# Kernel optimization log

Hardware: AMD Instinct MI355X
Metric: run time of the kernel (lower is better)

The kernel has to match this reference:

```python
import jax, jax.numpy as jnp
import numpy as np
from jax import lax

N, C1, C2, H, W = 4, 256, 256, 80, 80
CH = 128           # c_ = int(c2 * e)
G, KS = 1, 3       # groups, kernel_size
K = KS * KS        # sampling points per group
PAD, DIL = 1, 1
EPS_BN, EPS_LN = 1e-5, 1e-6


def conv_bn_silu(x, w, g, b, m, v, stride=1):
    # ultralytics Conv: conv(bias=False) + BatchNorm2d(eval) + SiLU
    pad = (w.shape[2] - 1) // 2
    y = lax.conv_general_dilated(x, w, (stride, stride), [(pad, pad), (pad, pad)],
                                 dimension_numbers=('NCHW', 'OIHW', 'NCHW'))
    s = g / jnp.sqrt(v + EPS_BN)
    y = y * s[None, :, None, None] + (b - m * s)[None, :, None, None]
    return jax.nn.silu(y)


def dcnv3_core(x, offset, mask):
    # x: (N,H,W,C) NHWC; offset: (N,H,W,G*K*2); mask: (N,H,W,G,K) softmaxed over K
    n, h, w, c = x.shape
    gc = c // G
    xp = jnp.pad(x, ((0, 0), (PAD, PAD), (PAD, PAD), (0, 0)))
    Hp, Wp = h + 2 * PAD, w + 2 * PAD
    base = (DIL * (KS - 1)) // 2
    # reference points (normalized by padded spatial size), stride 1
    ref_x = (jnp.arange(w, dtype=x.dtype) + base + 0.5) / Wp   # (W,)
    ref_y = (jnp.arange(h, dtype=x.dtype) + base + 0.5) / Hp   # (H,)
    gx = (jnp.arange(KS, dtype=x.dtype) * DIL - base) / Wp
    gy = (jnp.arange(KS, dtype=x.dtype) * DIL - base) / Hp
    grid_x = jnp.repeat(gx, KS)   # point p = i*KS + j -> x = gx[i]
    grid_y = jnp.tile(gy, KS)     # y = gy[j]  (torch meshgrid 'ij' ordering)
    off = offset.reshape(n, h, w, G, K, 2)
    loc_x = ref_x[None, None, :, None, None] + grid_x + off[..., 0] / Wp
    loc_y = ref_y[None, :, None, None, None] + grid_y + off[..., 1] / Hp
    # grid_sample align_corners=False: pixel = norm * size - 0.5
    px = loc_x * Wp - 0.5
    py = loc_y * Hp - 0.5
    x0 = jnp.floor(px); y0 = jnp.floor(py)
    lw, lh = px - x0, py - y0
    x0i, y0i = x0.astype(jnp.int32), y0.astype(jnp.int32)
    xv = jnp.transpose(xp.reshape(n, Hp * Wp, G, gc), (0, 2, 1, 3))  # (N,G,S,gc)
    tw = lambda a: jnp.transpose(a, (0, 3, 1, 2, 4))[..., None]      # (N,H,W,G,K)->(N,G,H,W,K,1)

    def gather(yi, xi):
        valid = ((xi >= 0) & (xi < Wp) & (yi >= 0) & (yi < Hp)).astype(x.dtype)
        idx = jnp.clip(yi, 0, Hp - 1) * Wp + jnp.clip(xi, 0, Wp - 1)
        idx = jnp.transpose(idx, (0, 3, 1, 2, 4)).reshape(n, G, h * w * K)
        v = jnp.take_along_axis(xv, idx[..., None], axis=2).reshape(n, G, h, w, K, gc)
        return v * tw(valid)   # zeros padding_mode

    out = (gather(y0i, x0i) * tw((1 - lh) * (1 - lw))
           + gather(y0i, x0i + 1) * tw((1 - lh) * lw)
           + gather(y0i + 1, x0i) * tw(lh * (1 - lw))
           + gather(y0i + 1, x0i + 1) * tw(lh * lw))   # (N,G,H,W,K,gc)
    m = jnp.transpose(mask, (0, 3, 1, 2, 4))[..., None]
    out = (out * m).sum(axis=4)                        # (N,G,H,W,gc)
    return jnp.transpose(out, (0, 2, 3, 1, 4)).reshape(n, h, w, c)


def forward(x, w1, g1, b1, m1, v1, w2, g2, b2, m2, v2,
            dw_w, dw_b, ln_g, ln_b, off_w, off_b, msk_w, msk_b,
            in_w, in_b, out_w, out_b, g3, b3, m3, v3):
    y = conv_bn_silu(x, w1, g1, b1, m1, v1)   # cv1: 3x3 Conv c1->c_
    y = conv_bn_silu(y, w2, g2, b2, m2, v2)   # cv2.conv: 1x1 Conv c_->c2
    t = jnp.transpose(y, (0, 2, 3, 1))        # NHWC
    x_proj = t @ in_w.T + in_b                # input_proj
    # dw_conv: depthwise 3x3 -> LayerNorm (channels_last) -> GELU
    dw = lax.conv_general_dilated(y, dw_w, (1, 1), [(1, 1), (1, 1)],
                                  dimension_numbers=('NCHW', 'OIHW', 'NCHW'),
                                  feature_group_count=C2)
    dw = jnp.transpose(dw, (0, 2, 3, 1)) + dw_b
    mu = dw.mean(-1, keepdims=True)
    var = ((dw - mu) ** 2).mean(-1, keepdims=True)
    dw = (dw - mu) / jnp.sqrt(var + EPS_LN) * ln_g + ln_b
    dw = jax.nn.gelu(dw, approximate=False)
    offset = dw @ off_w.T + off_b                                       # (N,H,W,G*K*2)
    mask = jax.nn.softmax((dw @ msk_w.T + msk_b).reshape(N, H, W, G, K), axis=-1)
    z = dcnv3_core(x_proj, offset, mask)
    z = z @ out_w.T + out_b                   # output_proj
    z = jnp.transpose(z, (0, 3, 1, 2))        # NCHW
    s = g3 / jnp.sqrt(v3 + EPS_BN)
    z = z * s[None, :, None, None] + (b3 - m3 * s)[None, :, None, None]
    z = jax.nn.silu(z)
    return x + z                              # shortcut (c1 == c2)


def setup_inputs():
    key = jax.random.key(0)
    ks = jax.random.split(key, 16)
    r = lambda k, s, sc=0.05: jax.random.normal(k, s, dtype=jnp.float32) * sc
    return {
        'x': jax.random.normal(ks[0], (N, C1, H, W), dtype=jnp.float32),
        'w1': r(ks[1], (CH, C1, 3, 3)),
        'g1': jnp.ones((CH,), jnp.float32), 'b1': jnp.zeros((CH,), jnp.float32),
        'm1': r(ks[2], (CH,), 0.1),
        'v1': jax.random.uniform(ks[3], (CH,), jnp.float32, 0.5, 1.5),
        'w2': r(ks[4], (C2, CH, 1, 1)),
        'g2': jnp.ones((C2,), jnp.float32), 'b2': jnp.zeros((C2,), jnp.float32),
        'm2': r(ks[5], (C2,), 0.1),
        'v2': jax.random.uniform(ks[6], (C2,), jnp.float32, 0.5, 1.5),
        'dw_w': r(ks[7], (C2, 1, 3, 3)), 'dw_b': jnp.zeros((C2,), jnp.float32),
        'ln_g': jnp.ones((C2,), jnp.float32), 'ln_b': jnp.zeros((C2,), jnp.float32),
        'off_w': r(ks[8], (G * K * 2, C2), 0.01), 'off_b': jnp.zeros((G * K * 2,), jnp.float32),
        'msk_w': r(ks[9], (G * K, C2), 0.01), 'msk_b': jnp.zeros((G * K,), jnp.float32),
        'in_w': r(ks[10], (C2, C2)), 'in_b': jnp.zeros((C2,), jnp.float32),
        'out_w': r(ks[11], (C2, C2)), 'out_b': jnp.zeros((C2,), jnp.float32),
        'g3': jnp.ones((C2,), jnp.float32), 'b3': jnp.zeros((C2,), jnp.float32),
        'm3': r(ks[12], (C2,), 0.1),
        'v3': jax.random.uniform(ks[13], (C2,), jnp.float32, 0.5, 1.5),
    }


def reference(x, w1, g1, b1, m1, v1, w2, g2, b2, m2, v2,
              dw_w, dw_b, ln_g, ln_b, off_w, off_b, msk_w, msk_b,
              in_w, in_b, out_w, out_b, g3, b3, m3, v3):
    return forward(x, w1, g1, b1, m1, v1, w2, g2, b2, m2, v2,
                   dw_w, dw_b, ln_g, ln_b, off_w, off_b, msk_w, msk_b,
                   in_w, in_b, out_w, out_b, g3, b3, m3, v3)
```

## Files before the change

### kernel.cpp

```cpp
#include <hip/hip_runtime.h>
#include <cmath>

#define TN 4
#define TC1 256
#define TCH 128
#define TC2 256
#define TH 80
#define TW 80
#define THP 82
#define TWP 84
#define NPIX (TN*TH*TW)

#define OFF_WBF   0
#define OFF_W2B   294912
#define OFF_INWB  327680
#define OFF_OUTWB 393216
#define OFF_DWT   458752
#define OFF_WCAT  461056
#define OFF_WCATB 467968
#define OFF_T1    468128
#define OFF_T2    468512
#define OFF_T3P   469024
#define OFF_XPAD  469504
#define OFF_Y1B   3997696
#define OFF_Y2N   7525888
#define OFF_DWN   469504
#define OFF_RAWN  10802688
#define OFF_ZN    11493888

typedef __attribute__((ext_vector_type(8))) short bf16x8;
typedef __attribute__((ext_vector_type(4))) float f32x4;

__device__ __forceinline__ float siluf(float v) { return v / (1.f + expf(-v)); }
__device__ __forceinline__ short rnbf(float f) {
  unsigned u = __float_as_uint(f);
  unsigned r = (u + 0x7fffu + ((u >> 16) & 1u)) >> 16;
  return (short)r;
}
__device__ __forceinline__ float bf2f(short s) {
  return __uint_as_float(((unsigned)(unsigned short)s) << 16);
}

__global__ __launch_bounds__(256) void k_prep(
    const float* __restrict__ w1, const float* __restrict__ g1, const float* __restrict__ b1,
    const float* __restrict__ m1, const float* __restrict__ v1,
    const float* __restrict__ w2, const float* __restrict__ g2, const float* __restrict__ b2,
    const float* __restrict__ m2, const float* __restrict__ v2,
    const float* __restrict__ dww, const float* __restrict__ offw, const float* __restrict__ offb,
    const float* __restrict__ mskw, const float* __restrict__ mskb,
    const float* __restrict__ inw, const float* __restrict__ outw, const float* __restrict__ outb,
    const float* __restrict__ g3, const float* __restrict__ b3,
    const float* __restrict__ m3, const float* __restrict__ v3,
    float* __restrict__ ws)
{
  int i = blockIdx.x * 256 + threadIdx.x;
  if (i < 294912) {
    int co = i / 2304; int r = i - co * 2304;
    int tap = r >> 8; int ci = r & 255; int ky = tap / 3; int kx = tap - ky * 3;
    float s = g1[co] * __frsqrt_rn(v1[co] + 1e-5f);
    ((short*)(ws + OFF_WBF))[i] = rnbf(w1[((co * TC1 + ci) * 3 + ky) * 3 + kx] * s);
    return;
  }
  i -= 294912;
  if (i < 32768) {
    int co = i >> 7; int ci = i & 127;
    float s = g2[co] * __frsqrt_rn(v2[co] + 1e-5f);
    ((short*)(ws + OFF_W2B))[i] = rnbf(w2[co * TCH + ci] * s);
    return;
  }
  i -= 32768;
  if (i < 65536) {
    int co = i >> 8; int ci = i & 255;
    ((short*)(ws + OFF_INWB))[i] = rnbf(inw[co * TC2 + ci]);
    return;
  }
  i -= 65536;
  if (i < 65536) {
    int co = i >> 8; int ci = i & 255;
    float s = g3[co] * __frsqrt_rn(v3[co] + 1e-5f);
    ((short*)(ws + OFF_OUTWB))[i] = rnbf(outw[co * TC2 + ci] * s);
    return;
  }
  i -= 65536;
  if (i < 2304) { int c = i & 255; int j = i >> 8; ws[OFF_DWT + i] = dww[c * 9 + j]; return; }
  i -= 2304;
  if (i < 8192) {
    int c = i & 255; int j = i >> 8;
    float v = 0.f;
    if (j < 18) v = offw[j * 256 + c];
    else if (j < 27) v = mskw[(j - 18) * 256 + c];
    ((short*)(ws + OFF_WCAT))[i] = rnbf(v);
    return;
  }
  i -= 8192;
  if (i < 27) { ws[OFF_WCATB + i] = (i < 18) ? offb[i] : mskb[i - 18]; return; }
  i -= 27;
  if (i < 128) { float s = g1[i] / sqrtf(v1[i] + 1e-5f); ws[OFF_T1 + i] = b1[i] - m1[i] * s; return; }
  i -= 128;
  if (i < 256) { float s = g2[i] / sqrtf(v2[i] + 1e-5f); ws[OFF_T2 + i] = b2[i] - m2[i] * s; return; }
  i -= 256;
  if (i < 256) { float s = g3[i] / sqrtf(v3[i] + 1e-5f); ws[OFF_T3P + i] = outb[i] * s + b3[i] - m3[i] * s; return; }
}

__global__ __launch_bounds__(256) void k_padx(const float* __restrict__ x, short* __restrict__ xpn)
{
  __shared__ short lds[80 * 40];
  int b = blockIdx.x;
  int cc = b & 7; int hp = (b >> 3) % THP; int n = b / (THP * 8);
  int c0 = cc * 32;
  int t = threadIdx.x;
  int h = hp - 1;
  bool hv = (h >= 0 && h < TH);
  if (hv) {
    for (int f = t; f < 640; f += 256) {
      int ci = f / 20; int w4 = (f - ci * 20) * 4;
      float4 xv = *(const float4*)(x + ((n * TC1 + c0 + ci) * TH + h) * TW + w4);
      lds[(w4 + 0) * 40 + ci] = rnbf(xv.x);
      lds[(w4 + 1) * 40 + ci] = rnbf(xv.y);
      lds[(w4 + 2) * 40 + ci] = rnbf(xv.z);
      lds[(w4 + 3) * 40 + ci] = rnbf(xv.w);
    }
  }
  __syncthreads();
  short* op = xpn + ((n * THP + hp) * TWP) * TC2 + c0;
  for (int g = t; g < 672; g += 256) {
    int ci4 = (g & 7) * 4; int wp = g >> 3;
    short4 v = {0, 0, 0, 0};
    if (hv && wp >= 1 && wp <= TW) v = *(const short4*)(&lds[(wp - 1) * 40 + ci4]);
    *(short4*)(op + wp * TC2 + ci4) = v;
  }
}

#define A_STR 40
__global__ __launch_bounds__(256) void k_cv1f(const short* __restrict__ xpn, const short* __restrict__ wbf,
                                              const float* __restrict__ t1v, short* __restrict__ y1b)
{
  __shared__ short As[2][128 * A_STR];
  __shared__ short Bs[2][64 * A_STR];

  int b = blockIdx.x;
  int wt = b % 5; b /= 5; int ht = b % 20; int n = b / 20;
  int w0 = wt * 16, h0 = ht * 4;

  int tid = threadIdx.x;
  int wave = tid >> 6, lane = tid & 63;
  int ln = lane & 15, q = lane >> 4;
  int coh = (wave & 1) * 64;
  int pxh = (wave >> 1) * 32;

  int arow = tid >> 1;
  int asub = (tid & 1) * 16;
  const short* abase = wbf + arow * 2304 + asub;
  int brow_r = tid >> 2;
  int bsub = (tid & 3) * 8;
  int bhr = brow_r >> 4, bwc = brow_r & 15;
  const short* bbase = xpn + ((n * THP + h0 + bhr) * TWP + (w0 + bwc)) * 256 + bsub;

  f32x4 acc[4][2];
#pragma unroll
  for (int i = 0; i < 4; ++i)
#pragma unroll
    for (int j = 0; j < 2; ++j) acc[i][j] = (f32x4){0.f, 0.f, 0.f, 0.f};

  bf16x8 ra0, ra1, rb;
  auto grab = [&](int c) {
    int tap = c >> 3;
    int ci0 = (c & 7) * 32;
    int ky = tap / 3, kx = tap - ky * 3;
    const short* ap = abase + tap * 256 + ci0;
    const short* bp = bbase + (ky * TWP + kx) * 256 + ci0;
    ra0 = *(const bf16x8*)(ap);
    ra1 = *(const bf16x8*)(ap + 8);
    rb  = *(const bf16x8*)(bp);
  };
  auto put = [&](int buf) {
    int oa = arow * A_STR + asub;
    *(bf16x8*)(&As[buf][oa])     = ra0;
    *(bf16x8*)(&As[buf][oa + 8]) = ra1;
    *(bf16x8*)(&Bs[buf][brow_r * A_STR + bsub]) = rb;
  };
  auto comp = [&](int buf) {
    bf16x8 af[4], bfv[2];
#pragma unroll
    for (int mt = 0; mt < 4; ++mt)
      af[mt] = *(const bf16x8*)(&As[buf][(coh + mt * 16 + ln) * A_STR + q * 8]);
#pragma unroll
    for (int nt = 0; nt < 2; ++nt)
      bfv[nt] = *(const bf16x8*)(&Bs[buf][(pxh + nt * 16 + ln) * A_STR + q * 8]);
#pragma unroll
    for (int mt = 0; mt < 4; ++mt)
#pragma unroll
      for (int nt = 0; nt < 2; ++nt)
        acc[mt][nt] = __builtin_amdgcn_mfma_f32_16x16x32_bf16(af[mt], bfv[nt], acc[mt][nt], 0, 0, 0);
  };

  grab(0);
  put(0);
  __syncthreads();
  for (int c = 0; c < 72; ++c) {
    if (c < 71) grab(c + 1);
    comp(c & 1);
    if (c < 71) {
      __syncthreads();
      put((c + 1) & 1);
      __syncthreads();
    }
  }

#pragma unroll
  for (int mt = 0; mt < 4; ++mt) {
    int co = coh + mt * 16 + q * 4;
    float t0 = t1v[co], t1 = t1v[co + 1], t2 = t1v[co + 2], t3 = t1v[co + 3];
#pragma unroll
    for (int nt = 0; nt < 2; ++nt) {
      int pl = pxh + nt * 16 + ln;
      int hr = pl >> 4, wc = pl & 15;
      int pix = (n * TH + h0 + hr) * TW + (w0 + wc);
      short4 p;
      p.x = rnbf(siluf(acc[mt][nt][0] + t0));
      p.y = rnbf(siluf(acc[mt][nt][1] + t1));
      p.z = rnbf(siluf(acc[mt][nt][2] + t2));
      p.w = rnbf(siluf(acc[mt][nt][3] + t3));
      *(short4*)(y1b + pix * TCH + co) = p;
    }
  }
}

__global__ __launch_bounds__(256) void k_cv2(const short* __restrict__ y1b, const short* __restrict__ w2b,
                                             const float* __restrict__ t2v, short* __restrict__ y2b)
{
  __shared__ short As[2][128 * A_STR];
  __shared__ short Bs[2][128 * A_STR];

  int b = blockIdx.x;
  int ch = b & 1; int pt = b >> 1;
  int co_base = ch * 128;
  int pix0 = pt * 128;

  int tid = threadIdx.x;
  int wave = tid >> 6, lane = tid & 63;
  int ln = lane & 15, q = lane >> 4;
  int coh = (wave & 1) * 64;
  int pxh = (wave >> 1) * 64;

  int srow = tid >> 1;
  int ssub = (tid & 1) * 16;
  const short* arow = w2b + (co_base + srow) * TCH + ssub;
  const short* brow = y1b + (pix0 + srow) * TCH + ssub;

  f32x4 acc[4][4];
#pragma unroll
  for (int i = 0; i < 4; ++i)
#pragma unroll
    for (int j = 0; j < 4; ++j) acc[i][j] = (f32x4){0.f, 0.f, 0.f, 0.f};

  bf16x8 ra0, ra1, rb0, rb1;
  auto grab = [&](int c) {
    const short* ap = arow + c * 32;
    const short* bp = brow + c * 32;
    ra0 = *(const bf16x8*)(ap);
    ra1 = *(const bf16x8*)(ap + 8);
    rb0 = *(const bf16x8*)(bp);
    rb1 = *(const bf16x8*)(bp + 8);
  };
  auto put = [&](int buf) {
    int o = srow * A_STR + ssub;
    *(bf16x8*)(&As[buf][o])     = ra0;
    *(bf16x8*)(&As[buf][o + 8]) = ra1;
    *(bf16x8*)(&Bs[buf][o])     = rb0;
    *(bf16x8*)(&Bs[buf][o + 8]) = rb1;
  };
  auto comp = [&](int buf) {
    bf16x8 af[4], bfv[4];
#pragma unroll
    for (int mt = 0; mt < 4; ++mt)
      af[mt] = *(const bf16x8*)(&As[buf][(coh + mt * 16 + ln) * A_STR + q * 8]);
#pragma unroll
    for (int nt = 0; nt < 4; ++nt)
      bfv[nt] = *(const bf16x8*)(&Bs[buf][(pxh + nt * 16 + ln) * A_STR + q * 8]);
#pragma unroll
    for (int mt = 0; mt < 4; ++mt)
#pragma unroll
      for (int nt = 0; nt < 4; ++nt)
        acc[mt][nt] = __builtin_amdgcn_mfma_f32_16x16x32_bf16(af[mt], bfv[nt], acc[mt][nt], 0, 0, 0);
  };

  const int NCH = TCH / 32;
  grab(0);
  put(0);
  __syncthreads();
  for (int c = 0; c < NCH; ++c) {
    if (c < NCH - 1) grab(c + 1);
    comp(c & 1);
    if (c < NCH - 1) {
      __syncthreads();
      put((c + 1) & 1);
      __syncthreads();
    }
  }

#pragma unroll
  for (int mt = 0; mt < 4; ++mt) {
    int co = co_base + coh + mt * 16 + q * 4;
    float t0 = t2v[co], t1 = t2v[co + 1], t2 = t2v[co + 2], t3 = t2v[co + 3];
#pragma unroll
    for (int nt = 0; nt < 4; ++nt) {
      int pix = pix0 + pxh + nt * 16 + ln;
      short4 p;
      p.x = rnbf(siluf(acc[mt][nt][0] + t0));
      p.y = rnbf(siluf(acc[mt][nt][1] + t1));
      p.z = rnbf(siluf(acc[mt][nt][2] + t2));
      p.w = rnbf(siluf(acc[mt][nt][3] + t3));
      *(short4*)(y2b + pix * TC2 + co) = p;
    }
  }
}

__global__ __launch_bounds__(256) void k_proj_in(const short* __restrict__ y2b, const short* __restrict__ inwb,
                                                 const float* __restrict__ inb, short* __restrict__ xproj)
{
  __shared__ short As[2][128 * A_STR];
  __shared__ short Bs[2][128 * A_STR];

  int b = blockIdx.x;
  int ch = b & 1; int pt = b >> 1;
  int co_base = ch * 128;
  int pix0 = pt * 128;

  int tid = threadIdx.x;
  int wave = tid >> 6, lane = tid & 63;
  int ln = lane & 15, q = lane >> 4;
  int coh = (wave & 1) * 64;
  int pxh = (wave >> 1) * 64;

  int srow = tid >> 1;
  int ssub = (tid & 1) * 16;
  const short* arow = inwb + (co_base + srow) * TC2 + ssub;
  const short* brow = y2b + (pix0 + srow) * TC2 + ssub;

  f32x4 acc[4][4];
#pragma unroll
  for (int i = 0; i < 4; ++i)
#pragma unroll
    for (int j = 0; j < 4; ++j) acc[i][j] = (f32x4){0.f, 0.f, 0.f, 0.f};

  bf16x8 ra0, ra1, rb0, rb1;
  auto grab = [&](int c) {
    const short* ap = arow + c * 32;
    const short* bp = brow + c * 32;
    ra0 = *(const bf16x8*)(ap);
    ra1 = *(const bf16x8*)(ap + 8);
    rb0 = *(const bf16x8*)(bp);
    rb1 = *(const bf16x8*)(bp + 8);
  };
  auto put = [&](int buf) {
    int o = srow * A_STR + ssub;
    *(bf16x8*)(&As[buf][o])     = ra0;
    *(bf16x8*)(&As[buf][o + 8]) = ra1;
    *(bf16x8*)(&Bs[buf][o])     = rb0;
    *(bf16x8*)(&Bs[buf][o + 8]) = rb1;
  };
  auto comp = [&](int buf) {
    bf16x8 af[4], bfv[4];
#pragma unroll
    for (int mt = 0; mt < 4; ++mt)
      af[mt] = *(const bf16x8*)(&As[buf][(coh + mt * 16 + ln) * A_STR + q * 8]);
#pragma unroll
    for (int nt = 0; nt < 4; ++nt)
      bfv[nt] = *(const bf16x8*)(&Bs[buf][(pxh + nt * 16 + ln) * A_STR + q * 8]);
#pragma unroll
    for (int mt = 0; mt < 4; ++mt)
#pragma unroll
      for (int nt = 0; nt < 4; ++nt)
        acc[mt][nt] = __builtin_amdgcn_mfma_f32_16x16x32_bf16(af[mt], bfv[nt], acc[mt][nt], 0, 0, 0);
  };

  const int NCH = TC2 / 32;
  grab(0);
  put(0);
  __syncthreads();
  for (int c = 0; c < NCH; ++c) {
    if (c < NCH - 1) grab(c + 1);
    comp(c & 1);
    if (c < NCH - 1) {
      __syncthreads();
      put((c + 1) & 1);
      __syncthreads();
    }
  }

#pragma unroll
  for (int mt = 0; mt < 4; ++mt) {
    int co = co_base + coh + mt * 16 + q * 4;
    float b0 = inb[co], b1 = inb[co + 1], b2 = inb[co + 2], b3 = inb[co + 3];
#pragma unroll
    for (int nt = 0; nt < 4; ++nt) {
      int pix = pix0 + pxh + nt * 16 + ln;
      short4 p;
      p.x = rnbf(acc[mt][nt][0] + b0);
      p.y = rnbf(acc[mt][nt][1] + b1);
      p.z = rnbf(acc[mt][nt][2] + b2);
      p.w = rnbf(acc[mt][nt][3] + b3);
      *(short4*)(xproj + pix * TC2 + co) = p;
    }
  }
}

__global__ __launch_bounds__(256) void k_dwln(const short* __restrict__ y2b, const float* __restrict__ dwt,
                                              const float* __restrict__ dwb, const float* __restrict__ lng,
                                              const float* __restrict__ lnb, short* __restrict__ dwo)
{
  int tid = threadIdx.x;
  int wave = tid >> 6, lane = tid & 63;
  int half = lane >> 5;
  int pix = blockIdx.x * 8 + wave * 2 + half;
  int w = pix % TW; int h = (pix / TW) % TH; int n = pix / (TH * TW);
  int c0 = (lane & 31) * 8;

  float v[8];
  {
    float4 b0 = *(const float4*)(dwb + c0);
    float4 b1 = *(const float4*)(dwb + c0 + 4);
    v[0] = b0.x; v[1] = b0.y; v[2] = b0.z; v[3] = b0.w;
    v[4] = b1.x; v[5] = b1.y; v[6] = b1.z; v[7] = b1.w;
  }
#pragma unroll
  for (int dy = 0; dy < 3; ++dy) {
#pragma unroll
    for (int dx = 0; dx < 3; ++dx) {
      int hh = h + dy - 1, ww = w + dx - 1;
      bool ok = (hh >= 0) & (hh < TH) & (ww >= 0) & (ww < TW);
      int off = ok ? (((n * TH + hh) * TW + ww) * TC2 + c0) : c0;
      bf16x8 yv = *(const bf16x8*)(y2b + off);
      float m = ok ? 1.f : 0.f;
      const float* wp = dwt + (dy * 3 + dx) * TC2 + c0;
      float4 w0 = *(const float4*)(wp);
      float4 w1 = *(const float4*)(wp + 4);
      v[0] += bf2f(yv[0]) * w0.x * m;
      v[1] += bf2f(yv[1]) * w0.y * m;
      v[2] += bf2f(yv[2]) * w0.z * m;
      v[3] += bf2f(yv[3]) * w0.w * m;
      v[4] += bf2f(yv[4]) * w1.x * m;
      v[5] += bf2f(yv[5]) * w1.y * m;
      v[6] += bf2f(yv[6]) * w1.z * m;
      v[7] += bf2f(yv[7]) * w1.w * m;
    }
  }
  float sv = 0.f, sq = 0.f;
#pragma unroll
  for (int i = 0; i < 8; ++i) { sv += v[i]; sq += v[i] * v[i]; }
#pragma unroll
  for (int o = 16; o > 0; o >>= 1) { sv += __shfl_xor(sv, o); sq += __shfl_xor(sq, o); }
  float mu = sv * (1.f / 256.f);
  float var = sq * (1.f / 256.f) - mu * mu;
  float rs = 1.f / sqrtf(var + 1e-6f);
  float4 g0 = *(const float4*)(lng + c0);
  float4 g1 = *(const float4*)(lng + c0 + 4);
  float4 bb0 = *(const float4*)(lnb + c0);
  float4 bb1 = *(const float4*)(lnb + c0 + 4);
  float gv[8] = {g0.x, g0.y, g0.z, g0.w, g1.x, g1.y, g1.z, g1.w};
  float bv[8] = {bb0.x, bb0.y, bb0.z, bb0.w, bb1.x, bb1.y, bb1.z, bb1.w};
  const float is2 = 0.70710678118654752f;
  bf16x8 o8;
#pragma unroll
  for (int i = 0; i < 8; ++i) {
    float nv = (v[i] - mu) * rs * gv[i] + bv[i];
    o8[i] = rnbf(0.5f * nv * (1.f + erff(nv * is2)));
  }
  *(bf16x8*)(dwo + pix * TC2 + c0) = o8;
}

__global__ __launch_bounds__(256) void k_offmask(const short* __restrict__ dwo, const short* __restrict__ wcatb16,
                                                 const float* __restrict__ wcatb, float* __restrict__ raw)
{
  int tid = threadIdx.x;
  int wave = tid >> 6, lane = tid & 63;
  int ln = lane & 15, q = lane >> 4;
  int pix0 = blockIdx.x * 64 + wave * 16;

  f32x4 acc0 = {0.f, 0.f, 0.f, 0.f};
  f32x4 acc1 = acc0;

  const short* a0p = wcatb16 + ln * 256 + q * 8;
  const short* a1p = wcatb16 + (16 + ln) * 256 + q * 8;
  const short* bp  = dwo + (pix0 + ln) * 256 + q * 8;
#pragma unroll
  for (int kk = 0; kk < 256; kk += 32) {
    bf16x8 bf = *(const bf16x8*)(bp + kk);
    bf16x8 a0 = *(const bf16x8*)(a0p + kk);
    bf16x8 a1 = *(const bf16x8*)(a1p + kk);
    acc0 = __builtin_amdgcn_mfma_f32_16x16x32_bf16(a0, bf, acc0, 0, 0, 0);
    acc1 = __builtin_amdgcn_mfma_f32_16x16x32_bf16(a1, bf, acc1, 0, 0, 0);
  }

  int pix = pix0 + ln;
#pragma unroll
  for (int r = 0; r < 4; ++r) {
    int j0 = q * 4 + r;
    raw[pix * 27 + j0] = acc0[r] + wcatb[j0];
    int j1 = 16 + j0;
    if (j1 < 27) raw[pix * 27 + j1] = acc1[r] + wcatb[j1];
  }
}

__global__ __launch_bounds__(256) void k_dcn(const short* __restrict__ xproj, const float* __restrict__ raw,
                                             short* __restrict__ z)
{
  __shared__ int2 sp[8][36];
  int tid = threadIdx.x;
  int pixbase = blockIdx.x * 8;

  for (int j = tid; j < 288; j += 256) {
    int pxl = j / 36, t = j - pxl * 36;
    int pix = pixbase + pxl;
    int w = pix % TW; int h = (pix / TW) % TH;
    const float* r = raw + pix * 27;
    int k = t >> 2, tap = t & 3;
    int tx = tap & 1, ty = tap >> 1;
    float mx = r[18];
#pragma unroll
    for (int kk = 1; kk < 9; ++kk) mx = fmaxf(mx, r[18 + kk]);
    float sum = 0.f, ek = 0.f;
#pragma unroll
    for (int kk = 0; kk < 9; ++kk) {
      float ee = expf(r[18 + kk] - mx);
      sum += ee;
      if (kk == k) ek = ee;
    }
    float mk = ek / sum;
    float px = (float)(w + k / 3) + r[2 * k];
    float py = (float)(h + k % 3) + r[2 * k + 1];
    float x0f = floorf(px), y0f = floorf(py);
    float lw = px - x0f, lh = py - y0f;
    int x0 = (int)x0f + tx, y0 = (int)y0f + ty;
    float wt = mk * (tx ? lw : 1.f - lw) * (ty ? lh : 1.f - lh);
    bool valid = (x0 >= 1) & (x0 <= TW) & (y0 >= 1) & (y0 <= TH);
    int2 pr;
    pr.x = valid ? (((y0 - 1) * TW + (x0 - 1)) * TC2) : 0;
    pr.y = valid ? __float_as_int(wt) : 0;
    sp[pxl][t] = pr;
  }
  __syncthreads();

  int wave = tid >> 6, lane = tid & 63;
  int half = lane >> 5;
  int pxl = wave * 2 + half;
  int pix = pixbase + pxl;
  int n = pix / (TH * TW);
  int c0 = (lane & 31) * 8;
  const short* xb = xproj + n * (TH * TW * TC2) + c0;

  float a[8] = {0.f, 0.f, 0.f, 0.f, 0.f, 0.f, 0.f, 0.f};
#pragma unroll
  for (int t = 0; t < 36; ++t) {
    int2 pr = sp[pxl][t];
    float wt = __int_as_float(pr.y);
    bf16x8 v = *(const bf16x8*)(xb + pr.x);
#pragma unroll
    for (int i = 0; i < 8; ++i) a[i] += wt * bf2f(v[i]);
  }
  bf16x8 o8;
#pragma unroll
  for (int i = 0; i < 8; ++i) o8[i] = rnbf(a[i]);
  *(bf16x8*)(z + pix * TC2 + c0) = o8;
}

__global__ __launch_bounds__(256) void k_proj_out(const short* __restrict__ zb, const short* __restrict__ outwb,
                                                  const float* __restrict__ t3p,
                                                  const float* __restrict__ x, float* __restrict__ out)
{
  __shared__ short As[2][128 * A_STR];
  __shared__ short Bs[2][128 * A_STR];

  int b = blockIdx.x;
  int ch = b & 1; int pt = b >> 1;
  int co_base = ch * 128;
  int pix0 = pt * 128;

  int tid = threadIdx.x;
  int wave = tid >> 6, lane = tid & 63;
  int ln = lane & 15, q = lane >> 4;
  int coh = (wave & 1) * 64;
  int pxh = (wave >> 1) * 64;

  int srow = tid >> 1;
  int ssub = (tid & 1) * 16;
  const short* arow = outwb + (co_base + srow) * TC2 + ssub;
  const short* brow = zb + (pix0 + srow) * TC2 + ssub;

  f32x4 acc[4][4];
#pragma unroll
  for (int i = 0; i < 4; ++i)
#pragma unroll
    for (int j = 0; j < 4; ++j) acc[i][j] = (f32x4){0.f, 0.f, 0.f, 0.f};

  bf16x8 ra0, ra1, rb0, rb1;
  auto grab = [&](int c) {
    const short* ap = arow + c * 32;
    const short* bp = brow + c * 32;
    ra0 = *(const bf16x8*)(ap);
    ra1 = *(const bf16x8*)(ap + 8);
    rb0 = *(const bf16x8*)(bp);
    rb1 = *(const bf16x8*)(bp + 8);
  };
  auto put = [&](int buf) {
    int o = srow * A_STR + ssub;
    *(bf16x8*)(&As[buf][o])     = ra0;
    *(bf16x8*)(&As[buf][o + 8]) = ra1;
    *(bf16x8*)(&Bs[buf][o])     = rb0;
    *(bf16x8*)(&Bs[buf][o + 8]) = rb1;
  };
  auto comp = [&](int buf) {
    bf16x8 af[4], bfv[4];
#pragma unroll
    for (int mt = 0; mt < 4; ++mt)
      af[mt] = *(const bf16x8*)(&As[buf][(coh + mt * 16 + ln) * A_STR + q * 8]);
#pragma unroll
    for (int nt = 0; nt < 4; ++nt)
      bfv[nt] = *(const bf16x8*)(&Bs[buf][(pxh + nt * 16 + ln) * A_STR + q * 8]);
#pragma unroll
    for (int mt = 0; mt < 4; ++mt)
#pragma unroll
      for (int nt = 0; nt < 4; ++nt)
        acc[mt][nt] = __builtin_amdgcn_mfma_f32_16x16x32_bf16(af[mt], bfv[nt], acc[mt][nt], 0, 0, 0);
  };

  const int NCH = TC2 / 32;
  grab(0);
  put(0);
  __syncthreads();
  for (int c = 0; c < NCH; ++c) {
    if (c < NCH - 1) grab(c + 1);
    comp(c & 1);
    if (c < NCH - 1) {
      __syncthreads();
      put((c + 1) & 1);
      __syncthreads();
    }
  }

#pragma unroll
  for (int mt = 0; mt < 4; ++mt) {
    int co = co_base + coh + mt * 16 + q * 4;
#pragma unroll
    for (int nt = 0; nt < 4; ++nt) {
      int pix = pix0 + pxh + nt * 16 + ln;
      int n = pix / (TH * TW);
      int hw = pix - n * (TH * TW);
#pragma unroll
      for (int r = 0; r < 4; ++r) {
        int addr = (n * TC2 + co + r) * (TH * TW) + hw;
        out[addr] = x[addr] + siluf(acc[mt][nt][r] + t3p[co + r]);
      }
    }
  }
}

extern "C" void kernel_launch(void* const* d_in, const int* in_sizes, int n_in,
                              void* d_out, int out_size, void* d_ws, size_t ws_size,
                              hipStream_t stream)
{
  const float* x    = (const float*)d_in[0];
  const float* w1   = (const float*)d_in[1];
  const float* g1   = (const float*)d_in[2];
  const float* b1   = (const float*)d_in[3];
  const float* m1   = (const float*)d_in[4];
  const float* v1   = (const float*)d_in[5];
  const float* w2   = (const float*)d_in[6];
  const float* g2   = (const float*)d_in[7];
  const float* b2   = (const float*)d_in[8];
  const float* m2   = (const float*)d_in[9];
  const float* v2   = (const float*)d_in[10];
  const float* dww  = (const float*)d_in[11];
  const float* dwb  = (const float*)d_in[12];
  const float* lng  = (const float*)d_in[13];
  const float* lnb  = (const float*)d_in[14];
  const float* offw = (const float*)d_in[15];
  const float* offb = (const float*)d_in[16];
  const float* mskw = (const float*)d_in[17];
  const float* mskb = (const float*)d_in[18];
  const float* inw  = (const float*)d_in[19];
  const float* inb  = (const float*)d_in[20];
  const float* outw = (const float*)d_in[21];
  const float* outb = (const float*)d_in[22];
  const float* g3   = (const float*)d_in[23];
  const float* b3   = (const float*)d_in[24];
  const float* m3   = (const float*)d_in[25];
  const float* v3   = (const float*)d_in[26];

  float* ws  = (float*)d_ws;
  float* out = (float*)d_out;

  short* xpn    = (short*)(ws + OFF_XPAD);
  short* wbf    = (short*)(ws + OFF_WBF);
  short* w2b    = (short*)(ws + OFF_W2B);
  short* inwb   = (short*)(ws + OFF_INWB);
  short* outwb  = (short*)(ws + OFF_OUTWB);
  short* wcat16 = (short*)(ws + OFF_WCAT);
  short* y1b    = (short*)(ws + OFF_Y1B);
  short* y2b    = (short*)(ws + OFF_Y2N);
  short* dwo    = (short*)(ws + OFF_DWN);
  float* raw    = ws + OFF_RAWN;
  short* zb     = (short*)(ws + OFF_ZN);
  short* xproj  = (short*)d_out;

  hipLaunchKernelGGL(k_prep, dim3(1836), dim3(256), 0, stream,
                     w1, g1, b1, m1, v1, w2, g2, b2, m2, v2,
                     dww, offw, offb, mskw, mskb, inw, outw, outb, g3, b3, m3, v3, ws);
  hipLaunchKernelGGL(k_padx,     dim3(TN * THP * 8), dim3(256), 0, stream, x, xpn);
  hipLaunchKernelGGL(k_cv1f,     dim3(400),   dim3(256), 0, stream, xpn, wbf, ws + OFF_T1, y1b);
  hipLaunchKernelGGL(k_cv2,      dim3(400),   dim3(256), 0, stream, y1b, w2b, ws + OFF_T2, y2b);
  hipLaunchKernelGGL(k_proj_in,  dim3(400),   dim3(256), 0, stream, y2b, inwb, inb, xproj);
  hipLaunchKernelGGL(k_dwln,     dim3(3200),  dim3(256), 0, stream, y2b, ws + OFF_DWT, dwb, lng, lnb, dwo);
  hipLaunchKernelGGL(k_offmask,  dim3(400),   dim3(256), 0, stream, dwo, wcat16, ws + OFF_WCATB, raw);
  hipLaunchKernelGGL(k_dcn,      dim3(3200),  dim3(256), 0, stream, xproj, raw, zb);
  hipLaunchKernelGGL(k_proj_out, dim3(400),   dim3(256), 0, stream, zb, outwb, ws + OFF_T3P, x, out);
}
```

Baseline: 278.2 us.

## Stage halo input tile once per channel chunk and read weights directly to registers

The 3x3 conv (cv1) kernel now loads a 6x18 halo tile of padded input into shared memory once per 32-channel chunk and reuses it across all 9 taps. Previously it loaded a shifted input tile for every tap-channel step. Weights bypass shared memory: each wave loads its 32 output-channel fragments straight from global into registers. This cuts 72 double-synchronized iterations to 8 and removes redundant input loads, at the cost of more registers (18 weight fragments held at once) and uncoalesced per-lane global weight reads.

```diff
diff --git a/kernel.cpp b/kernel.cpp
--- a/kernel.cpp
+++ b/kernel.cpp
@@ -131,12 +131,12 @@
   }
 }
 
-#define A_STR 40
+#define BH_STR 40
+#define BH_PIX 108
 __global__ __launch_bounds__(256) void k_cv1f(const short* __restrict__ xpn, const short* __restrict__ wbf,
                                               const float* __restrict__ t1v, short* __restrict__ y1b)
 {
-  __shared__ short As[2][128 * A_STR];
-  __shared__ short Bs[2][64 * A_STR];
+  __shared__ short Bh[2][BH_PIX * BH_STR];
 
   int b = blockIdx.x;
   int wt = b % 5; b /= 5; int ht = b % 20; int n = b / 20;
@@ -145,76 +145,77 @@
   int tid = threadIdx.x;
   int wave = tid >> 6, lane = tid & 63;
   int ln = lane & 15, q = lane >> 4;
-  int coh = (wave & 1) * 64;
-  int pxh = (wave >> 1) * 32;
-
-  int arow = tid >> 1;
-  int asub = (tid & 1) * 16;
-  const short* abase = wbf + arow * 2304 + asub;
-  int brow_r = tid >> 2;
-  int bsub = (tid & 3) * 8;
-  int bhr = brow_r >> 4, bwc = brow_r & 15;
-  const short* bbase = xpn + ((n * THP + h0 + bhr) * TWP + (w0 + bwc)) * 256 + bsub;
-
-  f32x4 acc[4][2];
-#pragma unroll
-  for (int i = 0; i < 4; ++i)
-#pragma unroll
-    for (int j = 0; j < 2; ++j) acc[i][j] = (f32x4){0.f, 0.f, 0.f, 0.f};
-
-  bf16x8 ra0, ra1, rb;
-  auto grab = [&](int c) {
-    int tap = c >> 3;
-    int ci0 = (c & 7) * 32;
-    int ky = tap / 3, kx = tap - ky * 3;
-    const short* ap = abase + tap * 256 + ci0;
-    const short* bp = bbase + (ky * TWP + kx) * 256 + ci0;
-    ra0 = *(const bf16x8*)(ap);
-    ra1 = *(const bf16x8*)(ap + 8);
-    rb  = *(const bf16x8*)(bp);
-  };
-  auto put = [&](int buf) {
-    int oa = arow * A_STR + asub;
-    *(bf16x8*)(&As[buf][oa])     = ra0;
-    *(bf16x8*)(&As[buf][oa + 8]) = ra1;
-    *(bf16x8*)(&Bs[buf][brow_r * A_STR + bsub]) = rb;
-  };
-  auto comp = [&](int buf) {
-    bf16x8 af[4], bfv[2];
-#pragma unroll
-    for (int mt = 0; mt < 4; ++mt)
-      af[mt] = *(const bf16x8*)(&As[buf][(coh + mt * 16 + ln) * A_STR + q * 8]);
-#pragma unroll
-    for (int nt = 0; nt < 2; ++nt)
-      bfv[nt] = *(const bf16x8*)(&Bs[buf][(pxh + nt * 16 + ln) * A_STR + q * 8]);
-#pragma unroll
-    for (int mt = 0; mt < 4; ++mt)
-#pragma unroll
-      for (int nt = 0; nt < 2; ++nt)
-        acc[mt][nt] = __builtin_amdgcn_mfma_f32_16x16x32_bf16(af[mt], bfv[nt], acc[mt][nt], 0, 0, 0);
-  };
-
-  grab(0);
-  put(0);
+  int co0 = wave * 32;
+
+  int u0 = tid, u1 = tid + 256;
+  int p0 = u0 >> 2, s0 = u0 & 3;
+  int p1 = u1 >> 2, s1 = u1 & 3;
+  int hh0 = p0 / 18, ww0 = p0 - hh0 * 18;
+  int hh1 = p1 / 18, ww1 = p1 - hh1 * 18;
+  const short* sb0 = xpn + ((n * THP + h0 + hh0) * TWP + (w0 + ww0)) * 256 + s0 * 8;
+  const short* sb1 = xpn + ((n * THP + h0 + hh1) * TWP + (w0 + ww1)) * 256 + s1 * 8;
+  bool hasu1 = (u1 < 432);
+  int d0 = p0 * BH_STR + s0 * 8;
+  int d1 = p1 * BH_STR + s1 * 8;
+
+  const short* abase = wbf + (co0 + ln) * 2304 + q * 8;
+
+  f32x4 acc[2][4];
+#pragma unroll
+  for (int i = 0; i < 2; ++i)
+#pragma unroll
+    for (int j = 0; j < 4; ++j) acc[i][j] = (f32x4){0.f, 0.f, 0.f, 0.f};
+
+  bf16x8 rb0 = *(const bf16x8*)(sb0);
+  bf16x8 rb1 = {0, 0, 0, 0, 0, 0, 0, 0};
+  if (hasu1) rb1 = *(const bf16x8*)(sb1);
+  *(bf16x8*)(&Bh[0][d0]) = rb0;
+  if (hasu1) *(bf16x8*)(&Bh[0][d1]) = rb1;
   __syncthreads();
-  for (int c = 0; c < 72; ++c) {
-    if (c < 71) grab(c + 1);
-    comp(c & 1);
-    if (c < 71) {
+
+  for (int cc = 0; cc < 8; ++cc) {
+    int cur = cc & 1;
+    bf16x8 af[9][2];
+#pragma unroll
+    for (int tap = 0; tap < 9; ++tap)
+#pragma unroll
+      for (int mt = 0; mt < 2; ++mt)
+        af[tap][mt] = *(const bf16x8*)(abase + (mt * 16) * 2304 + tap * 256 + cc * 32);
+    if (cc < 7) {
+      rb0 = *(const bf16x8*)(sb0 + (cc + 1) * 32);
+      if (hasu1) rb1 = *(const bf16x8*)(sb1 + (cc + 1) * 32);
+    }
+#pragma unroll
+    for (int tap = 0; tap < 9; ++tap) {
+      const int ky = tap / 3, kx = tap - (tap / 3) * 3;
+      bf16x8 bv[4];
+#pragma unroll
+      for (int nt = 0; nt < 4; ++nt) {
+        int pr = nt * 16 + ln;
+        int hr = pr >> 4, wc = pr & 15;
+        bv[nt] = *(const bf16x8*)(&Bh[cur][((hr + ky) * 18 + (wc + kx)) * BH_STR + q * 8]);
+      }
+#pragma unroll
+      for (int mt = 0; mt < 2; ++mt)
+#pragma unroll
+        for (int nt = 0; nt < 4; ++nt)
+          acc[mt][nt] = __builtin_amdgcn_mfma_f32_16x16x32_bf16(af[tap][mt], bv[nt], acc[mt][nt], 0, 0, 0);
+    }
+    if (cc < 7) {
+      *(bf16x8*)(&Bh[cur ^ 1][d0]) = rb0;
+      if (hasu1) *(bf16x8*)(&Bh[cur ^ 1][d1]) = rb1;
       __syncthreads();
-      put((c + 1) & 1);
-      __syncthreads();
-    }
-  }
-
-#pragma unroll
-  for (int mt = 0; mt < 4; ++mt) {
-    int co = coh + mt * 16 + q * 4;
+    }
+  }
+
+#pragma unroll
+  for (int mt = 0; mt < 2; ++mt) {
+    int co = co0 + mt * 16 + q * 4;
     float t0 = t1v[co], t1 = t1v[co + 1], t2 = t1v[co + 2], t3 = t1v[co + 3];
 #pragma unroll
-    for (int nt = 0; nt < 2; ++nt) {
-      int pl = pxh + nt * 16 + ln;
-      int hr = pl >> 4, wc = pl & 15;
+    for (int nt = 0; nt < 4; ++nt) {
+      int pr = nt * 16 + ln;
+      int hr = pr >> 4, wc = pr & 15;
       int pix = (n * TH + h0 + hr) * TW + (w0 + wc);
       short4 p;
       p.x = rnbf(siluf(acc[mt][nt][0] + t0));
@@ -226,6 +227,7 @@
   }
 }
 
+#define A_STR 40
 __global__ __launch_bounds__(256) void k_cv2(const short* __restrict__ y1b, const short* __restrict__ w2b,
                                              const float* __restrict__ t2v, short* __restrict__ y2b)
 {
```

After: 277.0 us. About the same (-0.4%).
